# Optimization experiments

Hardware: AMD Instinct MI355X
Metric: run time of the kernel (lower is better)

## Reference

```python
import jax, jax.numpy as jnp
import numpy as np

B, T, D, H = 4, 2048, 1024, 4
DK = D // H      # head_k_dim = 256
DV = D // H      # head_v_dim = 256
M = DK           # num_slots defaults to head_k_dim
GATE_NORM = 16.0
CLAMP_MIN, CLAMP_MAX = -32.0, 32.0
EPS = 1e-5
ROPE_BASE = 10000.0


def setup_inputs() -> dict:
    key = jax.random.key(0)
    ks = jax.random.split(key, 8)
    sd = 0.02  # stands in for xavier_uniform with gain 2**-2.5
    return {
        "hidden_states": jax.random.normal(ks[0], (B, T, D), jnp.float32),
        "q_w": jax.random.normal(ks[1], (D, D), jnp.float32) * sd,
        "k_w": jax.random.normal(ks[2], (D, D), jnp.float32) * sd,
        "v_w": jax.random.normal(ks[3], (D, D), jnp.float32) * sd,
        "g_w": jax.random.normal(ks[4], (D, D), jnp.float32) * sd,
        "s_w": jax.random.normal(ks[5], (D, H * M), jnp.float32) * sd,
        "sg_w": jax.random.normal(ks[6], (D, H), jnp.float32) * sd,
        "gn_w": jnp.ones((DV,), jnp.float32),
        "o_w": jax.random.normal(ks[7], (D, D), jnp.float32) * sd,
    }


def _rope(x):
    # x: [B, T, H, DK]; non-interleaved (flash-attn style) rotary, full head dim
    half = x.shape[-1] // 2
    inv = 1.0 / (ROPE_BASE ** (jnp.arange(half, dtype=jnp.float32) / half))
    ang = jnp.arange(x.shape[1], dtype=jnp.float32)[:, None] * inv[None, :]  # [T, half]
    cos = jnp.cos(ang)[None, :, None, :]
    sin = jnp.sin(ang)[None, :, None, :]
    x1, x2 = x[..., :half], x[..., half:]
    return jnp.concatenate([x1 * cos - x2 * sin, x2 * cos + x1 * sin], -1)


def _abc(q, k, v, s):
    # ABC linear attention with slot memory (fla chunk_abc semantics, g=None path).
    # q, k: [B,H,T,DK]; v: [B,H,T,DV]; s: [B,H,T,M] (clamped slot logits)
    scale = q.shape[-1] ** -0.5
    z = jax.lax.cumlogsumexp(s, axis=2)                    # running log-normalizer
    s_n = jnp.exp(s - z)                                   # normalized slot write weights
    g = jnp.exp(jnp.concatenate([z[:, :, :1], z[:, :, :-1]], 2) - z)  # per-step decay in (0,1]

    tm = lambda x: jnp.moveaxis(x, 2, 0)                   # time-major for scan

    # stage 1: key memory  hk[B,H,DK,M];  ok_t = scale * q_t @ hk_t
    def step_k(hk, inp):
        q_t, k_t, s_t, g_t = inp
        hk = hk * g_t[:, :, None, :] + k_t[..., None] * s_t[:, :, None, :]
        return hk, jnp.einsum('bhk,bhkm->bhm', q_t, hk)
    hk0 = jnp.zeros(q.shape[:2] + (q.shape[-1], s.shape[-1]), q.dtype)
    _, ok = jax.lax.scan(step_k, hk0, (tm(q * scale), tm(k), tm(s_n), tm(g)))

    qv = jax.nn.softmax(ok, axis=-1)                       # slot read weights, [T,B,H,M]

    # stage 2: value memory  hv[B,H,M,DV];  ov_t = qv_t @ hv_t
    def step_v(hv, inp):
        qv_t, v_t, s_t, g_t = inp
        hv = hv * g_t[..., None] + s_t[..., None] * v_t[:, :, None, :]
        return hv, jnp.einsum('bhm,bhmv->bhv', qv_t, hv)
    hv0 = jnp.zeros(v.shape[:2] + (s.shape[-1], v.shape[-1]), v.dtype)
    _, ov = jax.lax.scan(step_v, hv0, (qv, tm(v), tm(s_n), tm(g)))
    return jnp.moveaxis(ov, 0, 2)                          # [B,H,T,DV]


def reference(hidden_states, q_w, k_w, v_w, g_w, s_w, sg_w, gn_w, o_w):
    x = hidden_states
    q = (x @ q_w).reshape(B, T, H, DK)
    k = (x @ k_w).reshape(B, T, H, DK)
    v = (x @ v_w).reshape(B, T, H, DV).transpose(0, 2, 1, 3)       # [B,H,T,DV]
    q, k = _rope(q), _rope(k)
    q = q.transpose(0, 2, 1, 3)                                    # [B,H,T,DK]
    k = k.transpose(0, 2, 1, 3)

    s = (x @ s_w).reshape(B, T, H, M).transpose(0, 2, 1, 3)        # [B,H,T,M]
    s = jnp.clip(s, CLAMP_MIN, CLAMP_MAX)

    sg = jax.nn.log_sigmoid(x @ sg_w).transpose(0, 2, 1) / GATE_NORM  # [B,H,T]
    k = k * jnp.exp(jnp.cumsum(sg, axis=2))[..., None]

    o = _abc(q, k, v, s).transpose(0, 2, 1, 3)                     # [B,T,H,DV]

    g = (x @ g_w).reshape(B, T, H, DV)
    rms = o * jax.lax.rsqrt(jnp.mean(o * o, axis=-1, keepdims=True) + EPS) * gn_w
    o = (rms * g * jax.nn.sigmoid(g)).reshape(B, T, D)             # RMSNorm + swish gate
    return o @ o_w
```

## Files before the change

### kernel.cpp

```cpp
#include <hip/hip_runtime.h>
#include <hip/hip_bf16.h>
#include <stdint.h>
#include <stddef.h>
#include <math.h>

typedef __bf16 bf8_t __attribute__((ext_vector_type(8)));
typedef __bf16 bf4_t __attribute__((ext_vector_type(4)));
typedef float  f4_t  __attribute__((ext_vector_type(4)));
typedef unsigned int u32;

#define DEV static __device__ __forceinline__

namespace abc {
constexpr int B = 4, T = 2048, D = 1024, H = 4;
constexpr int BT = B * T;
constexpr int CH = 64;
constexpr int NC = T / CH;
constexpr int BH = B * H;
constexpr float SCALE = 0.0625f;
constexpr float GN = 16.0f;
constexpr float EPS = 1e-5f;
}

DEV f4_t mfma16(bf8_t a, bf8_t b, f4_t c) {
  return __builtin_amdgcn_mfma_f32_16x16x32_bf16(a, b, c, 0, 0, 0);
}

DEV void glds16(const void* g, void* l) {
  __builtin_amdgcn_global_load_lds(
      (const __attribute__((address_space(1))) u32*)g,
      (__attribute__((address_space(3))) u32*)l, 16, 0, 0);
}

DEV __bf16* slice_addr(__bf16* base, int row, int cg ) {
  return base + (((cg >> 2) * 2 + (row >> 7)) * 4096
               + ((((row & 127) << 2) | ((cg & 3) ^ (row & 3))) * 8));
}
DEV const __bf16* slice_addr(const __bf16* base, int row, int cg) {
  return base + (((cg >> 2) * 2 + (row >> 7)) * 4096
               + ((((row & 127) << 2) | ((cg & 3) ^ (row & 3))) * 8));
}

DEV void stage_lin(const __bf16* __restrict__ g, __bf16* lds, int tid) {
  #pragma unroll
  for (int i = 0; i < 2; i++)
    glds16(g + (size_t)(i * 256 + tid) * 8, lds + (i * 256 + (tid & ~63)) * 8);
}

template<int ROWS>
DEV void stage(const __bf16* __restrict__ g, int S ,
               __bf16* lds, int tid) {
  #pragma unroll
  for (int i = 0; i < ROWS / 64; i++) {
    int p = i * 256 + tid;
    int m = p >> 2;
    int q = (p & 3) ^ (m & 3);
    glds16(g + (size_t)m * S + q * 8, lds + (i * 256 + (tid & ~63)) * 8);
  }
}
DEV bf8_t bfrag(const __bf16* sl, int m, int quad) {
  return *reinterpret_cast<const bf8_t*>(sl + m * 32 + ((quad ^ (m & 3)) << 3));
}

DEV void ring_pre(int s) {
  if (s < 46)       asm volatile("s_waitcnt vmcnt(4)" ::: "memory");
  else if (s == 46) asm volatile("s_waitcnt vmcnt(2)" ::: "memory");
  else              asm volatile("s_waitcnt vmcnt(0)" ::: "memory");
  asm volatile("s_waitcnt lgkmcnt(0)" ::: "memory");
  asm volatile("s_barrier" ::: "memory");
}

__global__ __launch_bounds__(256)
void cvt_x_kernel(const float* __restrict__ x, __bf16* __restrict__ xb)
{
  const int idx = blockIdx.x * 256 + threadIdx.x;
  const float4* src = reinterpret_cast<const float4*>(x);
  float4 a = src[(size_t)idx * 2];
  float4 b = src[(size_t)idx * 2 + 1];
  bf8_t o;
  o[0] = (__bf16)a.x; o[1] = (__bf16)a.y; o[2] = (__bf16)a.z; o[3] = (__bf16)a.w;
  o[4] = (__bf16)b.x; o[5] = (__bf16)b.y; o[6] = (__bf16)b.z; o[7] = (__bf16)b.w;
  reinterpret_cast<bf8_t*>(xb)[idx] = o;
}

__global__ __launch_bounds__(256)
void cvt_w_kernel(const float* __restrict__ w0, const float* __restrict__ w1,
                  const float* __restrict__ w2, const float* __restrict__ w3,
                  const float* __restrict__ w4, const float* __restrict__ w5,
                  __bf16* __restrict__ wt)
{
  const int z = blockIdx.z;
  const float* W = (z == 0) ? w0 : (z == 1) ? w1 : (z == 2) ? w2
                 : (z == 3) ? w3 : (z == 4) ? w4 : w5;
  const int n0 = blockIdx.x * 64, k0 = blockIdx.y * 64;
  __shared__ __bf16 Ts[64][72];
  const int tid = threadIdx.x;
  #pragma unroll
  for (int i = 0; i < 4; i++) {
    int p = tid + 256 * i;
    int row = p >> 4, c4 = p & 15;
    float4 v = *reinterpret_cast<const float4*>(W + (size_t)(k0 + row) * 1024 + n0 + c4 * 4);
    Ts[c4 * 4 + 0][row] = (__bf16)v.x;
    Ts[c4 * 4 + 1][row] = (__bf16)v.y;
    Ts[c4 * 4 + 2][row] = (__bf16)v.z;
    Ts[c4 * 4 + 3][row] = (__bf16)v.w;
  }
  __syncthreads();
  #pragma unroll
  for (int i = 0; i < 2; i++) {
    int p = tid + 256 * i;
    int n = p >> 3, kq = p & 7;
    bf8_t o = *reinterpret_cast<const bf8_t*>(&Ts[n][kq * 8]);
    *reinterpret_cast<bf8_t*>(wt + (size_t)z * 1024 * 1024 + (size_t)(n0 + n) * 1024 + k0 + kq * 8) = o;
  }
}

template<bool OUT_BF16, int NZ>
__global__ __launch_bounds__(256)
void gemm_bt_kernel(const __bf16* __restrict__ A, const __bf16* __restrict__ BtB,
                    void* __restrict__ Cp)
{
  using namespace abc;
  constexpr int K = 1024;
  constexpr int NZC = 8 * NZ;
  const int bflat = blockIdx.x;
  const int xcd = bflat & 7;
  const int j = bflat >> 3;
  const int m_local = j / NZC;
  const int nz = j % NZC;
  const int nt = nz & 7, z = nz >> 3;
  const int m0 = (xcd * 8 + m_local) * 128;
  const int n0 = nt * 128;
  const __bf16* Bt = BtB + (size_t)z * K * 1024;
  __shared__ __bf16 As[128 * 64];
  __shared__ __bf16 Bs[128 * 64];
  const int tid = threadIdx.x;
  const int lane = tid & 63, wvid = tid >> 6;
  const int wr = wvid >> 1, wc = wvid & 1;
  const int quad = lane >> 4, l16 = lane & 15;
  const f4_t fzero = {0.f, 0.f, 0.f, 0.f};
  f4_t acc[4][4];
  #pragma unroll
  for (int i = 0; i < 4; i++)
    #pragma unroll
    for (int j2 = 0; j2 < 4; j2++) acc[i][j2] = fzero;

  const int chunk_row = tid >> 3;
  const int chunk_col = tid & 7;
  for (int k0 = 0; k0 < K; k0 += 64) {
    __syncthreads();
    #pragma unroll
    for (int i = 0; i < 4; i++) {
      glds16(A + (size_t)(m0 + i * 32 + chunk_row) * K + k0 + chunk_col * 8,
             &As[(size_t)(i * 256 + wvid * 64) * 8]);
    }
    #pragma unroll
    for (int i = 0; i < 4; i++) {
      glds16(Bt + (size_t)(n0 + i * 32 + chunk_row) * K + k0 + chunk_col * 8,
             &Bs[(size_t)(i * 256 + wvid * 64) * 8]);
    }
    __syncthreads();
    #pragma unroll
    for (int ks = 0; ks < 2; ks++) {
      bf8_t af[4], bfv[4];
      #pragma unroll
      for (int i = 0; i < 4; i++)
        af[i] = *reinterpret_cast<const bf8_t*>(
            &As[(size_t)(wr * 64 + i * 16 + l16) * 64 + ks * 32 + quad * 8]);
      #pragma unroll
      for (int j2 = 0; j2 < 4; j2++)
        bfv[j2] = *reinterpret_cast<const bf8_t*>(
            &Bs[(size_t)(wc * 64 + j2 * 16 + l16) * 64 + ks * 32 + quad * 8]);
      #pragma unroll
      for (int i = 0; i < 4; i++)
        #pragma unroll
        for (int j2 = 0; j2 < 4; j2++)
          acc[i][j2] = mfma16(af[i], bfv[j2], acc[i][j2]);
    }
  }
  const int crow = m0 + wr * 64, ccol = n0 + wc * 64;
  if (OUT_BF16) {
    __bf16* C = (__bf16*)Cp + (size_t)z * BT * 1024;
    #pragma unroll
    for (int i = 0; i < 4; i++)
      #pragma unroll
      for (int j2 = 0; j2 < 4; j2++)
        #pragma unroll
        for (int r = 0; r < 4; r++)
          C[(size_t)(crow + i * 16 + quad * 4 + r) * 1024 + ccol + j2 * 16 + l16] =
              (__bf16)acc[i][j2][r];
  } else {
    float* C = (float*)Cp;
    #pragma unroll
    for (int i = 0; i < 4; i++)
      #pragma unroll
      for (int j2 = 0; j2 < 4; j2++)
        #pragma unroll
        for (int r = 0; r < 4; r++)
          C[(size_t)(crow + i * 16 + quad * 4 + r) * 1024 + ccol + j2 * 16 + l16] =
              acc[i][j2][r];
  }
}

__global__ __launch_bounds__(256)
void sg_kernel(const float* __restrict__ x, const float* __restrict__ sgw,
               float* __restrict__ sgl)
{
  using namespace abc;
  const int wvid = threadIdx.x >> 6, lane = threadIdx.x & 63;
  const int bt = blockIdx.x * 4 + wvid;
  const float* xr = x + (size_t)bt * 1024;
  float a0 = 0, a1 = 0, a2 = 0, a3 = 0;
  #pragma unroll 4
  for (int u = 0; u < 16; u++) {
    int i = u * 64 + lane;
    float xv = xr[i];
    float4 w = *reinterpret_cast<const float4*>(sgw + (size_t)i * 4);
    a0 += xv * w.x; a1 += xv * w.y; a2 += xv * w.z; a3 += xv * w.w;
  }
  #pragma unroll
  for (int off = 32; off > 0; off >>= 1) {
    a0 += __shfl_down(a0, off);
    a1 += __shfl_down(a1, off);
    a2 += __shfl_down(a2, off);
    a3 += __shfl_down(a3, off);
  }
  if (lane == 0) {
    const int b = bt >> 11, t = bt & (T - 1);
    float r[4] = {a0, a1, a2, a3};
    #pragma unroll
    for (int h = 0; h < 4; h++) {
      float v = r[h];
      float ls = fminf(v, 0.f) - log1pf(expf(-fabsf(v)));
      sgl[(size_t)(b * 4 + h) * T + t] = ls * (1.0f / GN);
    }
  }
}

__global__ __launch_bounds__(256)
void scan_kernel(const float* __restrict__ sgl, float* __restrict__ sgc)
{
  using namespace abc;
  const int bh = blockIdx.x;
  const float* in = sgl + (size_t)bh * T;
  float* out = sgc + (size_t)bh * T;
  __shared__ float part[256];
  const int tid = threadIdx.x;
  float v[8]; float s = 0.f;
  #pragma unroll
  for (int i = 0; i < 8; i++) { v[i] = in[tid * 8 + i]; s += v[i]; }
  part[tid] = s;
  __syncthreads();
  for (int off = 1; off < 256; off <<= 1) {
    float a = (tid >= off) ? part[tid - off] : 0.f;
    __syncthreads();
    part[tid] += a;
    __syncthreads();
  }
  float run = (tid > 0) ? part[tid - 1] : 0.f;
  #pragma unroll
  for (int i = 0; i < 8; i++) { run += v[i]; out[tid * 8 + i] = run; }
}

__global__ __launch_bounds__(256)
void prep_kernel(__bf16* __restrict__ q, __bf16* __restrict__ k,
                 __bf16* __restrict__ s, const float* __restrict__ sgc)
{
  using namespace abc;
  const int bt = blockIdx.x;
  const int b = bt >> 11, t = bt & (T - 1);
  const int tid = threadIdx.x;
  const size_t ro = (size_t)bt * 1024;
  #pragma unroll
  for (int i = 0; i < 2; i++) {
    int p = tid + 256 * i;
    int h = p >> 7, d = p & 127;
    float inv = expf(-(float)d * (9.210340371976184f / 128.0f));
    float ang = (float)t * inv;
    float sn, cs;
    sincosf(ang, &sn, &cs);
    size_t base = ro + (size_t)h * 256 + d;
    float q1 = (float)q[base], q2 = (float)q[base + 128];
    q[base]       = (__bf16)(q1 * cs - q2 * sn);
    q[base + 128] = (__bf16)(q2 * cs + q1 * sn);
    float dec = expf(sgc[(size_t)(b * 4 + h) * T + t]);
    float k1 = (float)k[base], k2 = (float)k[base + 128];
    k[base]       = (__bf16)((k1 * cs - k2 * sn) * dec);
    k[base + 128] = (__bf16)((k2 * cs + k1 * sn) * dec);
  }
  #pragma unroll
  for (int i = 0; i < 4; i++) {
    int e = tid + 256 * i;
    float v = (float)s[ro + e];
    v = fminf(fmaxf(v, -32.f), 32.f);
    s[ro + e] = (__bf16)expf(v);
  }
}

template<bool NEW0, bool NEW1>
__global__ __launch_bounds__(256)
void transpose_kernel(const __bf16* __restrict__ s0, const __bf16* __restrict__ s1,
                      __bf16* __restrict__ d0, __bf16* __restrict__ d1)
{
  using namespace abc;
  const int c = blockIdx.x, bh = blockIdx.y, z = blockIdx.z;
  const int b = bh >> 2, h = bh & 3;
  const size_t R = (size_t)b * T + (size_t)c * CH;
  const int F = h * 256;
  const __bf16* src = z ? s1 : s0;
  __bf16* dst = (z ? d1 : d0) + ((size_t)bh * NC + c) * (256 * 64);
  const bool NEWL = z ? NEW1 : NEW0;
  __shared__ __bf16 L[256 * 64];
  const int tid = threadIdx.x;
  #pragma unroll
  for (int j = 0; j < 8; j++) {
    int p = tid + 256 * j;
    int t = p >> 5, fc = p & 31;
    bf8_t v = *reinterpret_cast<const bf8_t*>(src + (R + t) * 1024 + F + fc * 8);
    const int sw = ((t >> 3) ^ (fc & 7)) * 8 + (t & 7);
    #pragma unroll
    for (int u = 0; u < 8; u++)
      L[(fc * 8 + u) * 64 + sw] = v[u];
  }
  __syncthreads();
  #pragma unroll
  for (int j = 0; j < 8; j++) {
    int p = tid + 256 * j;
    int f = p >> 3, q = p & 7;
    int phys = q ^ ((f >> 3) & 7);
    bf8_t o = *reinterpret_cast<const bf8_t*>(&L[f * 64 + phys * 8]);
    __bf16* daddr = NEWL ? slice_addr(dst, f, q)
                         : dst + (size_t)f * 64 + q * 8;
    *reinterpret_cast<bf8_t*>(daddr) = o;
  }
}

__global__ __launch_bounds__(256)
void chunkstate_kernel(const __bf16* __restrict__ KT, const __bf16* __restrict__ VT,
                       const __bf16* __restrict__ AT,
                       __bf16* __restrict__ HKc, __bf16* __restrict__ HVc,
                       float* __restrict__ csA)
{
  using namespace abc;
  const int c = blockIdx.x, bh = blockIdx.y, part = blockIdx.z;
  const size_t TB = ((size_t)bh * NC + c) * (256 * 64);
  const bool isHV = part >= 2;
  const int p2 = part & 1;
  const __bf16* Aop = (isHV ? VT : AT) + TB;
  const __bf16* Bop = (isHV ? AT : KT) + TB;
  const int tid = threadIdx.x;
  if (part == 2) {
    float ssum = 0.f;
    #pragma unroll
    for (int u = 0; u < 8; u++) {
      bf8_t v = *reinterpret_cast<const bf8_t*>(slice_addr(AT + TB, tid, u));
      #pragma unroll
      for (int w = 0; w < 8; w++) ssum += (float)v[w];
    }
    csA[((size_t)bh * NC + c) * 256 + tid] = ssum;
  }
  const int lane = tid & 63, wvid = tid >> 6;
  const int quad = lane >> 4, l16 = lane & 15;
  const int row0 = p2 * 128 + wvid * 32;
  const f4_t fzero = {0.f, 0.f, 0.f, 0.f};
  f4_t acc[2][16];
  #pragma unroll
  for (int a = 0; a < 2; a++)
    #pragma unroll
    for (int ct = 0; ct < 16; ct++) acc[a][ct] = fzero;
  #pragma unroll
  for (int ks = 0; ks < 2; ks++) {
    const int cg = ks * 4 + quad;
    bf8_t af0 = *reinterpret_cast<const bf8_t*>(slice_addr(Aop, row0 + l16, cg));
    bf8_t af1 = *reinterpret_cast<const bf8_t*>(slice_addr(Aop, row0 + 16 + l16, cg));
    #pragma unroll
    for (int ct = 0; ct < 16; ct++) {
      bf8_t bv;
      if (isHV)
        bv = *reinterpret_cast<const bf8_t*>(slice_addr(Bop, ct * 16 + l16, cg));
      else
        bv = *reinterpret_cast<const bf8_t*>(Bop + (size_t)(ct * 16 + l16) * 64 + ks * 32 + quad * 8);
      acc[0][ct] = mfma16(af0, bv, acc[0][ct]);
      acc[1][ct] = mfma16(af1, bv, acc[1][ct]);
    }
  }
  __bf16* out = (isHV ? HVc : HKc) + ((size_t)bh * NC + c) * 65536;
  #pragma unroll
  for (int rt = 0; rt < 2; rt++)
    #pragma unroll
    for (int ct = 0; ct < 16; ct++)
      #pragma unroll
      for (int r = 0; r < 4; r++) {
        const int mg = row0 + rt * 16 + quad * 4 + r;
        const int n  = ct * 16 + l16;
        *(slice_addr(out, mg, n >> 3) + (n & 7)) = (__bf16)acc[rt][ct][r];
      }
}

__global__ __launch_bounds__(256)
void prefix_state_kernel(__bf16* __restrict__ HKc, __bf16* __restrict__ HVc)
{
  using namespace abc;
  const int bh = blockIdx.y;
  __bf16* base = (blockIdx.z ? HVc : HKc) + (size_t)bh * NC * 65536;
  const int e = (blockIdx.x * 256 + threadIdx.x) * 8;
  float run[8];
  #pragma unroll
  for (int u = 0; u < 8; u++) run[u] = 0.f;
  #pragma unroll 4
  for (int c = 0; c < NC; c++) {
    __bf16* p = base + (size_t)c * 65536 + e;
    bf8_t v = *reinterpret_cast<const bf8_t*>(p);
    bf8_t o;
    #pragma unroll
    for (int u = 0; u < 8; u++) { o[u] = (__bf16)run[u]; run[u] += (float)v[u]; }
    *reinterpret_cast<bf8_t*>(p) = o;
  }
}

__global__ __launch_bounds__(256)
void prefix_csa_kernel(float* __restrict__ csA)
{
  using namespace abc;
  const int bh = blockIdx.x, m = threadIdx.x;
  float run = 0.f;
  for (int c = 0; c < NC; c++) {
    float* p = csA + ((size_t)bh * NC + c) * 256 + m;
    float v = *p; *p = run; run += v;
  }
}

__global__ __launch_bounds__(256)
void attn_kernel(const __bf16* __restrict__ qg, const __bf16* __restrict__ kg,
                 const __bf16* __restrict__ ag, const __bf16* __restrict__ gg,
                 const __bf16* __restrict__ ATp, const __bf16* __restrict__ VTp,
                 const __bf16* __restrict__ HKp, const __bf16* __restrict__ HVp,
                 const float* __restrict__ Zp, const float* __restrict__ gnw,
                 __bf16* __restrict__ yout)
{
  using namespace abc;
  const int c = blockIdx.x, bh = blockIdx.y;
  const int b = bh >> 2, h = bh & 3;
  const size_t R = (size_t)b * T + (size_t)c * CH;
  const int F = h * 256;
  const int tid = threadIdx.x;
  const int lane = tid & 63, wvid = tid >> 6;
  const int quad = lane >> 4, l16 = lane & 15;

  __shared__ __bf16 ST[4][4096];
  __shared__ __bf16 Ws[64][264];
  __shared__ __bf16 S1s[64][72];
  __shared__ float zs[256];
  __shared__ float gns[256];

  const __bf16* atb = ATp + ((size_t)bh * NC + c) * (256 * 64);
  const __bf16* vtb = VTp + ((size_t)bh * NC + c) * (256 * 64);
  const __bf16* hkb = HKp + ((size_t)bh * NC + c) * 65536;
  const __bf16* hvb = HVp + ((size_t)bh * NC + c) * 65536;
  const __bf16* kbase = kg + R * 1024 + F;
  const __bf16* abase = ag + R * 1024 + F;

  zs[tid] = Zp[((size_t)bh * NC + c) * 256 + tid];
  gns[tid] = gnw[tid];
  __syncthreads();

  const __bf16* qrow = qg + (R + wvid * 16 + l16) * 1024 + F;
  bf8_t aq[8];
  #pragma unroll
  for (int ks = 0; ks < 8; ks++)
    aq[ks] = *reinterpret_cast<const bf8_t*>(qrow + ks * 32 + quad * 8);

  const f4_t fzero = {0.f, 0.f, 0.f, 0.f};

  auto issue = [&](int s) {
    if (s >= 48) return;
    __bf16* buf = &ST[s & 3][0];
    if (s < 4) {
      stage<64>(kbase + (2 * s) * 32, 1024, buf, tid);
      stage<64>(kbase + (2 * s + 1) * 32, 1024, buf + 2048, tid);
    } else if (s < 8) {
      stage_lin(atb + (s - 4) * 4096, buf, tid);
    } else if (s < 24) {
      stage_lin(hkb + (s - 8) * 4096, buf, tid);
    } else if (s < 28) {
      int j = s - 24;
      stage<64>(abase + (2 * j) * 32, 1024, buf, tid);
      stage<64>(abase + (2 * j + 1) * 32, 1024, buf + 2048, tid);
    } else if (s < 44) {
      stage_lin(hvb + (s - 28) * 4096, buf, tid);
    } else {
      stage_lin(vtb + (s - 44) * 4096, buf, tid);
    }
  };

  issue(0); issue(1); issue(2);

  f4_t s1a[4];
  #pragma unroll
  for (int it = 0; it < 4; it++) s1a[it] = fzero;
  #pragma unroll
  for (int j = 0; j < 4; j++) {
    ring_pre(j);
    issue(j + 3);
    const __bf16* sl = &ST[j & 3][0];
    #pragma unroll
    for (int ks2 = 0; ks2 < 2; ks2++) {
      bf8_t a = aq[2 * j + ks2];
      const __bf16* sb = sl + ks2 * 2048;
      #pragma unroll
      for (int it = 0; it < 4; it++)
        s1a[it] = mfma16(a, bfrag(sb, it * 16 + l16, quad), s1a[it]);
    }
  }
  #pragma unroll
  for (int it = 0; it < 4; it++)
    #pragma unroll
    for (int r = 0; r < 4; r++) {
      int tl = wvid * 16 + quad * 4 + r;
      int il = it * 16 + l16;
      S1s[tl][il] = (il <= tl) ? (__bf16)s1a[it][r] : (__bf16)0.0f;
    }

  f4_t aok[16], acum[16];
  #pragma unroll
  for (int mt = 0; mt < 16; mt++) { aok[mt] = fzero; acum[mt] = fzero; }
  #pragma unroll
  for (int j = 0; j < 4; j++) {
    int s = 4 + j, iks = j >> 1, rh = j & 1;
    ring_pre(s);
    issue(s + 3);
    const __bf16* sl = &ST[s & 3][0];
    bf8_t s1f = *reinterpret_cast<const bf8_t*>(&S1s[wvid * 16 + l16][iks * 32 + quad * 8]);
    bf8_t lf;
    #pragma unroll
    for (int u = 0; u < 8; u++)
      lf[u] = (iks * 32 + quad * 8 + u <= wvid * 16 + l16) ? (__bf16)1.0f : (__bf16)0.0f;
    #pragma unroll
    for (int m8 = 0; m8 < 8; m8++) {
      bf8_t bfa = bfrag(sl, m8 * 16 + l16, quad);
      aok[rh * 8 + m8]  = mfma16(s1f, bfa, aok[rh * 8 + m8]);
      acum[rh * 8 + m8] = mfma16(lf,  bfa, acum[rh * 8 + m8]);
    }
  }

  #pragma unroll
  for (int j = 0; j < 16; j++) {
    int s = 8 + j, ks = j >> 1, rh = j & 1;
    ring_pre(s);
    issue(s + 3);
    const __bf16* sl = &ST[s & 3][0];
    #pragma unroll
    for (int m8 = 0; m8 < 8; m8++) {
      bf8_t bv = bfrag(sl, m8 * 16 + l16, quad);
      aok[rh * 8 + m8] = mfma16(aq[ks], bv, aok[rh * 8 + m8]);
    }
  }

  #pragma unroll
  for (int r = 0; r < 4; r++) {
    float ovv[16], sa[16];
    float mx = -3.0e38f;
    #pragma unroll
    for (int mt = 0; mt < 16; mt++) {
      sa[mt] = zs[mt * 16 + l16] + acum[mt][r];
      ovv[mt] = SCALE * aok[mt][r] / sa[mt];
      mx = fmaxf(mx, ovv[mt]);
    }
    #pragma unroll
    for (int off = 1; off < 16; off <<= 1) mx = fmaxf(mx, __shfl_xor(mx, off));
    float se = 0.f;
    #pragma unroll
    for (int mt = 0; mt < 16; mt++) { ovv[mt] = __expf(ovv[mt] - mx); se += ovv[mt]; }
    #pragma unroll
    for (int off = 1; off < 16; off <<= 1) se += __shfl_xor(se, off);
    float inv = 1.0f / se;
    int tl = wvid * 16 + quad * 4 + r;
    #pragma unroll
    for (int mt = 0; mt < 16; mt++)
      Ws[tl][mt * 16 + l16] = (__bf16)(ovv[mt] * inv / sa[mt]);
  }

  f4_t pacc[4];
  #pragma unroll
  for (int it = 0; it < 4; it++) pacc[it] = fzero;
  #pragma unroll
  for (int j = 0; j < 4; j++) {
    int s = 24 + j;
    ring_pre(s);
    issue(s + 3);
    const __bf16* sl = &ST[s & 3][0];
    #pragma unroll
    for (int ks2 = 0; ks2 < 2; ks2++) {
      int ks = 2 * j + ks2;
      bf8_t wf = *reinterpret_cast<const bf8_t*>(&Ws[wvid * 16 + l16][ks * 32 + quad * 8]);
      const __bf16* sb = sl + ks2 * 2048;
      #pragma unroll
      for (int it = 0; it < 4; it++)
        pacc[it] = mfma16(wf, bfrag(sb, it * 16 + l16, quad), pacc[it]);
    }
  }
  #pragma unroll
  for (int it = 0; it < 4; it++)
    #pragma unroll
    for (int r = 0; r < 4; r++) {
      int tl = wvid * 16 + quad * 4 + r;
      int il = it * 16 + l16;
      S1s[tl][il] = (il <= tl) ? (__bf16)pacc[it][r] : (__bf16)0.0f;
    }

  f4_t oacc[16];
  #pragma unroll
  for (int vt = 0; vt < 16; vt++) oacc[vt] = fzero;
  #pragma unroll
  for (int j = 0; j < 16; j++) {
    int s = 28 + j, ks = j >> 1, rh = j & 1;
    ring_pre(s);
    issue(s + 3);
    const __bf16* sl = &ST[s & 3][0];
    bf8_t wf = *reinterpret_cast<const bf8_t*>(&Ws[wvid * 16 + l16][ks * 32 + quad * 8]);
    #pragma unroll
    for (int v8 = 0; v8 < 8; v8++) {
      bf8_t bv = bfrag(sl, v8 * 16 + l16, quad);
      oacc[rh * 8 + v8] = mfma16(wf, bv, oacc[rh * 8 + v8]);
    }
  }

  #pragma unroll
  for (int j = 0; j < 4; j++) {
    int s = 44 + j, iks = j >> 1, rh = j & 1;
    ring_pre(s);
    issue(s + 3);
    const __bf16* sl = &ST[s & 3][0];
    bf8_t pf = *reinterpret_cast<const bf8_t*>(&S1s[wvid * 16 + l16][iks * 32 + quad * 8]);
    #pragma unroll
    for (int v8 = 0; v8 < 8; v8++) {
      bf8_t bvt = bfrag(sl, v8 * 16 + l16, quad);
      oacc[rh * 8 + v8] = mfma16(pf, bvt, oacc[rh * 8 + v8]);
    }
  }

  #pragma unroll
  for (int r = 0; r < 4; r++) {
    float ss = 0.f;
    #pragma unroll
    for (int vt = 0; vt < 16; vt++) ss += oacc[vt][r] * oacc[vt][r];
    #pragma unroll
    for (int off = 1; off < 16; off <<= 1) ss += __shfl_xor(ss, off);
    float rinv = rsqrtf(ss * (1.0f / 256.0f) + EPS);
    int tl = wvid * 16 + quad * 4 + r;
    const __bf16* grow = gg + (R + tl) * 1024 + F;
    __bf16* yrow = yout + (R + tl) * 1024 + F;
    #pragma unroll
    for (int vt = 0; vt < 16; vt++) {
      int v = vt * 16 + l16;
      float gvl = (float)grow[v];
      float yv = oacc[vt][r] * rinv * gns[v] * gvl / (1.0f + __expf(-gvl));
      yrow[v] = (__bf16)yv;
    }
  }
}

extern "C" void kernel_launch(void* const* d_in, const int* in_sizes, int n_in,
                              void* d_out, int out_size, void* d_ws, size_t ws_size,
                              hipStream_t stream) {
  using namespace abc;
  (void)in_sizes; (void)n_in; (void)out_size; (void)ws_size;
  const float* x    = (const float*)d_in[0];
  const float* q_w  = (const float*)d_in[1];
  const float* k_w  = (const float*)d_in[2];
  const float* v_w  = (const float*)d_in[3];
  const float* g_w  = (const float*)d_in[4];
  const float* s_w  = (const float*)d_in[5];
  const float* sg_w = (const float*)d_in[6];
  const float* gn_w = (const float*)d_in[7];
  const float* o_w  = (const float*)d_in[8];
  float* out = (float*)d_out;

  char* ws = (char*)d_ws;
  const size_t PROJ = (size_t)BT * 1024;
  __bf16* proj = (__bf16*)ws;
  __bf16* q_bf = proj + 0 * PROJ;
  __bf16* k_bf = proj + 1 * PROJ;
  __bf16* v_bf = proj + 2 * PROJ;
  __bf16* g_bf = proj + 3 * PROJ;
  __bf16* a_bf = proj + 4 * PROJ;
  __bf16* xb   = proj + 5 * PROJ;
  float* sgl = (float*)(ws + (size_t)96 * 1024 * 1024);
  float* sgc = sgl + (size_t)BH * T;
  float* csA = sgc + (size_t)BH * T;
  __bf16* HKc = (__bf16*)(ws + (size_t)97 * 1024 * 1024);
  __bf16* HVc = HKc + (size_t)BH * NC * 65536;
  __bf16* wt  = (__bf16*)(ws + (size_t)225 * 1024 * 1024);
  __bf16* KT  = (__bf16*)(ws + (size_t)237 * 1024 * 1024);
  __bf16* VT  = xb;
  __bf16* AT  = v_bf;
  __bf16* y_bf = KT;

  dim3 blk(256);
  cvt_w_kernel<<<dim3(16, 16, 6), blk, 0, stream>>>(q_w, k_w, v_w, g_w, s_w, o_w, wt);
  cvt_x_kernel<<<dim3(BT * 1024 / (256 * 8)), blk, 0, stream>>>(x, xb);
  gemm_bt_kernel<true, 5><<<dim3(64 * 8 * 5), blk, 0, stream>>>(xb, wt, proj);
  sg_kernel<<<dim3(BT / 4), blk, 0, stream>>>(x, sg_w, sgl);
  scan_kernel<<<dim3(BH), blk, 0, stream>>>(sgl, sgc);
  prep_kernel<<<dim3(BT), blk, 0, stream>>>(q_bf, k_bf, a_bf, sgc);
  transpose_kernel<false, true><<<dim3(NC, BH, 2), blk, 0, stream>>>(k_bf, v_bf, KT, VT);
  transpose_kernel<true, true><<<dim3(NC, BH, 1), blk, 0, stream>>>(a_bf, a_bf, AT, AT);
  chunkstate_kernel<<<dim3(NC, BH, 4), blk, 0, stream>>>(KT, VT, AT, HKc, HVc, csA);
  prefix_state_kernel<<<dim3(32, BH, 2), blk, 0, stream>>>(HKc, HVc);
  prefix_csa_kernel<<<dim3(BH), blk, 0, stream>>>(csA);
  attn_kernel<<<dim3(NC, BH), blk, 0, stream>>>(
      q_bf, k_bf, a_bf, g_bf, AT, VT, HKc, HVc, csA, gn_w, y_bf);
  gemm_bt_kernel<false, 1><<<dim3(64 * 8), blk, 0, stream>>>(
      y_bf, wt + (size_t)5 * 1024 * 1024, out);
}
```

Measured before the change: 499.6 us.

## Replace 128x128 GEMM with double-buffered 256x256 tile GEMM using 512 threads

Both projection GEMMs move from 128x128 tiles with 256 threads and a synchronous single LDS buffer to 256x256 tiles with 512 threads (8 waves), double-buffered LDS with swizzled layout, and loads for the next k-slice issued before the MFMAs of the current one. Raised setprio around the MFMA block favors compute issue. The goal is higher arithmetic intensity and overlap of global-to-LDS copies with compute. The cost is more registers (128 accumulators per lane) and fewer blocks, so the output GEMM now launches only 128 workgroups on a chip with 256 CUs, which may underfill the device.

Result: slower. 515.9 us (+3.3%).

```diff
diff --git a/kernel.cpp b/kernel.cpp
--- a/kernel.cpp
+++ b/kernel.cpp
@@ -70,6 +70,15 @@
   asm volatile("s_barrier" ::: "memory");
 }
 
+DEV void stage_g(const __bf16* __restrict__ g, int S, __bf16* lds, int tid) {
+  int m = tid >> 2;
+  int q = (tid & 3) ^ ((m >> 1) & 3);
+  glds16(g + (size_t)m * S + q * 8, lds + (tid & ~63) * 8);
+}
+DEV bf8_t bfrag_g(const __bf16* sl, int m, int quad) {
+  return *reinterpret_cast<const bf8_t*>(sl + m * 32 + (((quad ^ (m >> 1)) & 3) << 3));
+}
+
 __global__ __launch_bounds__(256)
 void cvt_x_kernel(const float* __restrict__ x, __bf16* __restrict__ xb)
 {
@@ -116,89 +125,94 @@
 }
 
 template<bool OUT_BF16, int NZ>
-__global__ __launch_bounds__(256)
-void gemm_bt_kernel(const __bf16* __restrict__ A, const __bf16* __restrict__ BtB,
+__global__ __launch_bounds__(512, 2)
+void gemm256_kernel(const __bf16* __restrict__ A, const __bf16* __restrict__ BtB,
                     void* __restrict__ Cp)
 {
   using namespace abc;
   constexpr int K = 1024;
-  constexpr int NZC = 8 * NZ;
+  constexpr int NZT = 4 * NZ;
   const int bflat = blockIdx.x;
   const int xcd = bflat & 7;
   const int j = bflat >> 3;
-  const int m_local = j / NZC;
-  const int nz = j % NZC;
-  const int nt = nz & 7, z = nz >> 3;
-  const int m0 = (xcd * 8 + m_local) * 128;
-  const int n0 = nt * 128;
+  const int m_local = j / NZT;
+  const int nz = j % NZT;
+  const int nt = nz & 3, z = nz >> 2;
+  const int m0 = (xcd * 4 + m_local) * 256;
+  const int n0 = nt * 256;
   const __bf16* Bt = BtB + (size_t)z * K * 1024;
-  __shared__ __bf16 As[128 * 64];
-  __shared__ __bf16 Bs[128 * 64];
+
+  __shared__ __bf16 LA[2][4][4096];
+  __shared__ __bf16 LB[2][4][4096];
+
   const int tid = threadIdx.x;
-  const int lane = tid & 63, wvid = tid >> 6;
-  const int wr = wvid >> 1, wc = wvid & 1;
+  const int lane = tid & 63, wv = tid >> 6;
+  const int wr = wv >> 2, wc = wv & 3;
   const int quad = lane >> 4, l16 = lane & 15;
   const f4_t fzero = {0.f, 0.f, 0.f, 0.f};
-  f4_t acc[4][4];
-  #pragma unroll
-  for (int i = 0; i < 4; i++)
-    #pragma unroll
-    for (int j2 = 0; j2 < 4; j2++) acc[i][j2] = fzero;
-
-  const int chunk_row = tid >> 3;
-  const int chunk_col = tid & 7;
-  for (int k0 = 0; k0 < K; k0 += 64) {
-    __syncthreads();
-    #pragma unroll
-    for (int i = 0; i < 4; i++) {
-      glds16(A + (size_t)(m0 + i * 32 + chunk_row) * K + k0 + chunk_col * 8,
-             &As[(size_t)(i * 256 + wvid * 64) * 8]);
-    }
-    #pragma unroll
-    for (int i = 0; i < 4; i++) {
-      glds16(Bt + (size_t)(n0 + i * 32 + chunk_row) * K + k0 + chunk_col * 8,
-             &Bs[(size_t)(i * 256 + wvid * 64) * 8]);
-    }
-    __syncthreads();
+  f4_t acc[8][4];
+  #pragma unroll
+  for (int fr = 0; fr < 8; fr++)
+    #pragma unroll
+    for (int fc = 0; fc < 4; fc++) acc[fr][fc] = fzero;
+
+  auto issue4 = [&](int kt, int ks) {
+    const int db = kt & 1;
+    const int kcol = kt * 64 + ks * 32;
+    stage_g(A  + (size_t)(m0 +   0) * K + kcol, K, &LA[db][0 + ks][0], tid);
+    stage_g(A  + (size_t)(m0 + 128) * K + kcol, K, &LA[db][2 + ks][0], tid);
+    stage_g(Bt + (size_t)(n0 +   0) * K + kcol, K, &LB[db][0 + ks][0], tid);
+    stage_g(Bt + (size_t)(n0 + 128) * K + kcol, K, &LB[db][2 + ks][0], tid);
+  };
+
+  issue4(0, 0); issue4(0, 1);
+
+  for (int kt = 0; kt < 16; kt++) {
+    const int db = kt & 1;
+    const bool last = (kt == 15);
     #pragma unroll
     for (int ks = 0; ks < 2; ks++) {
-      bf8_t af[4], bfv[4];
-      #pragma unroll
-      for (int i = 0; i < 4; i++)
-        af[i] = *reinterpret_cast<const bf8_t*>(
-            &As[(size_t)(wr * 64 + i * 16 + l16) * 64 + ks * 32 + quad * 8]);
-      #pragma unroll
-      for (int j2 = 0; j2 < 4; j2++)
-        bfv[j2] = *reinterpret_cast<const bf8_t*>(
-            &Bs[(size_t)(wc * 64 + j2 * 16 + l16) * 64 + ks * 32 + quad * 8]);
-      #pragma unroll
-      for (int i = 0; i < 4; i++)
+      if (last && ks == 1) asm volatile("s_waitcnt vmcnt(0)\ns_barrier" ::: "memory");
+      else                 asm volatile("s_waitcnt vmcnt(4)\ns_barrier" ::: "memory");
+      bf8_t af[8], bfv[4];
+      #pragma unroll
+      for (int fr = 0; fr < 8; fr++)
+        af[fr] = bfrag_g(&LA[db][wr * 2 + ks][0], fr * 16 + l16, quad);
+      #pragma unroll
+      for (int fc = 0; fc < 4; fc++)
+        bfv[fc] = bfrag_g(&LB[db][(wc >> 1) * 2 + ks][0], (wc & 1) * 64 + fc * 16 + l16, quad);
+      if (!last) issue4(kt + 1, ks);
+      __builtin_amdgcn_s_setprio(1);
+      #pragma unroll
+      for (int fr = 0; fr < 8; fr++)
         #pragma unroll
-        for (int j2 = 0; j2 < 4; j2++)
-          acc[i][j2] = mfma16(af[i], bfv[j2], acc[i][j2]);
-    }
-  }
-  const int crow = m0 + wr * 64, ccol = n0 + wc * 64;
+        for (int fc = 0; fc < 4; fc++)
+          acc[fr][fc] = mfma16(af[fr], bfv[fc], acc[fr][fc]);
+      __builtin_amdgcn_s_setprio(0);
+    }
+  }
+
+  const int crow = m0 + wr * 128, ccol = n0 + wc * 64;
   if (OUT_BF16) {
     __bf16* C = (__bf16*)Cp + (size_t)z * BT * 1024;
     #pragma unroll
-    for (int i = 0; i < 4; i++)
-      #pragma unroll
-      for (int j2 = 0; j2 < 4; j2++)
+    for (int fr = 0; fr < 8; fr++)
+      #pragma unroll
+      for (int fc = 0; fc < 4; fc++)
         #pragma unroll
         for (int r = 0; r < 4; r++)
-          C[(size_t)(crow + i * 16 + quad * 4 + r) * 1024 + ccol + j2 * 16 + l16] =
-              (__bf16)acc[i][j2][r];
+          C[(size_t)(crow + fr * 16 + quad * 4 + r) * 1024 + ccol + fc * 16 + l16] =
+              (__bf16)acc[fr][fc][r];
   } else {
     float* C = (float*)Cp;
     #pragma unroll
-    for (int i = 0; i < 4; i++)
-      #pragma unroll
-      for (int j2 = 0; j2 < 4; j2++)
+    for (int fr = 0; fr < 8; fr++)
+      #pragma unroll
+      for (int fc = 0; fc < 4; fc++)
         #pragma unroll
         for (int r = 0; r < 4; r++)
-          C[(size_t)(crow + i * 16 + quad * 4 + r) * 1024 + ccol + j2 * 16 + l16] =
-              acc[i][j2][r];
+          C[(size_t)(crow + fr * 16 + quad * 4 + r) * 1024 + ccol + fc * 16 + l16] =
+              acc[fr][fc][r];
   }
 }
 
@@ -697,9 +711,10 @@
   __bf16* y_bf = KT;
 
   dim3 blk(256);
+  dim3 blk512(512);
   cvt_w_kernel<<<dim3(16, 16, 6), blk, 0, stream>>>(q_w, k_w, v_w, g_w, s_w, o_w, wt);
   cvt_x_kernel<<<dim3(BT * 1024 / (256 * 8)), blk, 0, stream>>>(x, xb);
-  gemm_bt_kernel<true, 5><<<dim3(64 * 8 * 5), blk, 0, stream>>>(xb, wt, proj);
+  gemm256_kernel<true, 5><<<dim3(32 * 4 * 5), blk512, 0, stream>>>(xb, wt, proj);
   sg_kernel<<<dim3(BT / 4), blk, 0, stream>>>(x, sg_w, sgl);
   scan_kernel<<<dim3(BH), blk, 0, stream>>>(sgl, sgc);
   prep_kernel<<<dim3(BT), blk, 0, stream>>>(q_bf, k_bf, a_bf, sgc);
@@ -710,6 +725,6 @@
   prefix_csa_kernel<<<dim3(BH), blk, 0, stream>>>(csA);
   attn_kernel<<<dim3(NC, BH), blk, 0, stream>>>(
       q_bf, k_bf, a_bf, g_bf, AT, VT, HKc, HVc, csA, gn_w, y_bf);
-  gemm_bt_kernel<false, 1><<<dim3(64 * 8), blk, 0, stream>>>(
+  gemm256_kernel<false, 1><<<dim3(32 * 4), blk512, 0, stream>>>(
       y_bf, wt + (size_t)5 * 1024 * 1024, out);
 }
```
